# Optimization experiments

Hardware: AMD Instinct MI355X
Metric: run time of the kernel (lower is better)

The kernel has to match this reference:

```python
import jax, jax.numpy as jnp
import numpy as np

B, T, C, V = 4, 2048, 1024, 50257


def setup_inputs() -> dict:
    key = jax.random.key(0)
    k1, k2, k3 = jax.random.split(key, 3)
    x = jax.random.normal(k1, (B, T, C), dtype=jnp.float32)
    y = jax.random.randint(k2, (B, T), 0, V, dtype=jnp.int64)
    # nn.Linear(C, V): weight [V, C], bias [V]
    W = jax.random.normal(k3, (V, C), dtype=jnp.float32) * (1.0 / np.sqrt(C))
    b = jnp.zeros((V,), dtype=jnp.float32)
    return {"x": x, "y": y, "W": W, "b": b}


def reference(x, y, W, b):
    # logits: [B*T, V]
    logits = jnp.einsum("btc,vc->btv", x, W).reshape(B * T, V) + b
    labels = y.reshape(-1)  # [B*T]
    logp = jax.nn.log_softmax(logits, axis=-1)
    nll = -jnp.take_along_axis(logp, labels[:, None], axis=-1)[:, 0]
    return jnp.mean(nll)
```

## Files before the change

### kernel.cpp

```cpp
#include <hip/hip_runtime.h>


#define M_TOT 8192
#define K_TOT 1024
#define V_TOT 50257
#define NVB   197
#define NPAD  (NVB * 256)
#define PSTRIDE (NVB * 2)
#define KB    (K_TOT / 64)
#define GSTRIDE ((long)KB * 64 * 32)

typedef __attribute__((ext_vector_type(8)))  int   int8v;
typedef __attribute__((ext_vector_type(16))) float floatx16;

__device__ __forceinline__ int f4_to_fp8x4(float4 v) {
  int r = __builtin_amdgcn_cvt_pk_fp8_f32(v.x, v.y, 0, false);
  r = __builtin_amdgcn_cvt_pk_fp8_f32(v.z, v.w, r, true);
  return r;
}

__global__ __launch_bounds__(256) void pack_kernel(
    const float* __restrict__ src, char* __restrict__ dst, int nrows) {
  const int kb = blockIdx.x, g = blockIdx.y;
  const int i = threadIdx.x;
  const int r = i >> 3, seg = i & 7;
  const int srow = g * 32 + r;
  int lo = 0, hi = 0;
  if (srow < nrows) {
    const float4* s = (const float4*)(src + (long)srow * K_TOT + kb * 64 + seg * 8);
    lo = f4_to_fp8x4(s[0]);
    hi = f4_to_fp8x4(s[1]);
  }
  const int h = seg >> 2;
  char* d = dst + (((long)(g * KB + kb) * 64 + h * 32 + r) * 32 + (seg & 3) * 8);
  *(int2*)d = make_int2(lo, hi);
}

__global__ __launch_bounds__(256, 2) void gemm_lse_kernel(
    const char* __restrict__ pW, const char* __restrict__ pX,
    const float* __restrict__ bias, float* __restrict__ psum) {
  const int tid  = threadIdx.x;
  const int wave = tid >> 6;
  const int lane = tid & 63;
  const int wv   = wave >> 1;
  const int wb   = wave & 1;
  const int mblk = blockIdx.x;
  const int vblk = blockIdx.y;

  const char* pa[4];
  const char* pb[2];
#pragma unroll
  for (int tv = 0; tv < 4; ++tv)
    pa[tv] = pW + (long)(vblk * 8 + wv * 4 + tv) * GSTRIDE + (long)lane * 32;
#pragma unroll
  for (int tn = 0; tn < 2; ++tn)
    pb[tn] = pX + (long)(mblk * 4 + wb * 2 + tn) * GSTRIDE + (long)lane * 32;

  floatx16 acc[4][2] = {};
#pragma unroll 2
  for (int kb = 0; kb < KB; ++kb) {
    const int off = kb * 2048;
    int8v a[4], b[2];
#pragma unroll
    for (int tn = 0; tn < 2; ++tn) b[tn] = *(const int8v*)(pb[tn] + off);
#pragma unroll
    for (int tv = 0; tv < 4; ++tv) a[tv] = *(const int8v*)(pa[tv] + off);
#pragma unroll
    for (int tv = 0; tv < 4; ++tv)
#pragma unroll
      for (int tn = 0; tn < 2; ++tn)
        acc[tv][tn] = __builtin_amdgcn_mfma_scale_f32_32x32x64_f8f6f4(
            a[tv], b[tn], acc[tv][tn], 0, 0, 0, 0x7F7F7F7F, 0, 0x7F7F7F7F);
  }

  const int half = lane >> 5, l32 = lane & 31;
  const int vbase = vblk * 256 + wv * 128 + 4 * half;
  float s0 = 0.0f, s1 = 0.0f;
#pragma unroll
  for (int tv = 0; tv < 4; ++tv) {
#pragma unroll
    for (int reg = 0; reg < 16; ++reg) {
      int v = vbase + tv * 32 + (reg & 3) + 8 * (reg >> 2);
      float bv = (v < V_TOT) ? bias[v] : -1e30f;
      s0 += __expf(acc[tv][0][reg] + bv);
      s1 += __expf(acc[tv][1][reg] + bv);
    }
  }
  s0 += __shfl_xor(s0, 32, 64);
  s1 += __shfl_xor(s1, 32, 64);
  if (half == 0) {
    int m = mblk * 128 + wb * 64 + l32;
    long base = (long)m * PSTRIDE + vblk * 2 + wv;
    psum[base] = s0;
    psum[base + (long)32 * PSTRIDE] = s1;
  }
}

__global__ __launch_bounds__(256) void finalize_kernel(
    const float* __restrict__ psum, const float* __restrict__ x,
    const float* __restrict__ W, const float* __restrict__ b,
    const int* __restrict__ y, float* __restrict__ loss) {
  const int wave = threadIdx.x >> 6;
  const int lane = threadIdx.x & 63;
  const int r = blockIdx.x * 4 + wave;

  const float* ps = psum + (long)r * PSTRIDE;
  float s = 0.0f;
  for (int j = lane; j < PSTRIDE; j += 64) s += ps[j];
#pragma unroll
  for (int o = 1; o < 64; o <<= 1) s += __shfl_xor(s, o, 64);

  int label = y[r];
  const float4* xr = (const float4*)(x + (long)r * K_TOT);
  const float4* wr = (const float4*)(W + (long)label * K_TOT);
  float d = 0.0f;
  for (int j = lane; j < K_TOT / 4; j += 64) {
    float4 a = xr[j], w = wr[j];
    d += a.x * w.x + a.y * w.y + a.z * w.z + a.w * w.w;
  }
#pragma unroll
  for (int o = 1; o < 64; o <<= 1) d += __shfl_xor(d, o, 64);

  if (lane == 0) loss[r] = logf(s) - d - b[label];
}

__global__ __launch_bounds__(256) void reduce_kernel(
    const float* __restrict__ loss, float* __restrict__ out) {
  const int tid = threadIdx.x;
  float s = 0.0f;
  for (int j = tid; j < M_TOT; j += 256) s += loss[j];
#pragma unroll
  for (int o = 1; o < 64; o <<= 1) s += __shfl_xor(s, o, 64);
  __shared__ float wsum[4];
  if ((tid & 63) == 0) wsum[tid >> 6] = s;
  __syncthreads();
  if (tid == 0)
    out[0] = (wsum[0] + wsum[1] + wsum[2] + wsum[3]) * (1.0f / (float)M_TOT);
}

extern "C" void kernel_launch(void* const* d_in, const int* in_sizes, int n_in,
                              void* d_out, int out_size, void* d_ws, size_t ws_size,
                              hipStream_t stream) {
  (void)in_sizes; (void)n_in; (void)out_size; (void)ws_size;
  const float* x = (const float*)d_in[0];
  const int*   y = (const int*)d_in[1];
  const float* W = (const float*)d_in[2];
  const float* b = (const float*)d_in[3];
  float* out = (float*)d_out;

  char* ws = (char*)d_ws;
  const size_t PX_BYTES = (size_t)M_TOT * K_TOT;
  const size_t PW_BYTES = (size_t)NPAD * K_TOT;
  const size_t PS_BYTES = (size_t)M_TOT * PSTRIDE * 4;
  char*  pX   = ws;
  char*  pW   = ws + PX_BYTES;
  float* psum = (float*)(ws + PX_BYTES + PW_BYTES);
  float* loss = (float*)(ws + PX_BYTES + PW_BYTES + PS_BYTES);

  pack_kernel<<<dim3(KB, M_TOT / 32), 256, 0, stream>>>(x, pX, M_TOT);
  pack_kernel<<<dim3(KB, NPAD / 32), 256, 0, stream>>>(W, pW, V_TOT);
  gemm_lse_kernel<<<dim3(M_TOT / 128, NVB), 256, 0, stream>>>(pW, pX, b, psum);
  finalize_kernel<<<M_TOT / 4, 256, 0, stream>>>(psum, x, W, b, y, loss);
  reduce_kernel<<<1, 256, 0, stream>>>(loss, out);
}
```

Before: 736.6 us.

## Stage GEMM operands through swizzled double-buffered LDS with 512-thread blocks

The GEMM kernel previously had each wave load its fp8 fragments straight from global memory. It now stages A and B tiles into double-buffered LDS using global_load_lds, and the pack kernel writes an XOR-swizzled layout so the LDS reads avoid bank conflicts. Blocks grow to 512 threads covering 256 rows of M, so each loaded W tile is reused across more rows. Bias values are cached in LDS, and wave priority is raised around the MFMAs. In exchange it adds 128KB+ of LDS per block, which limits occupancy, plus extra barriers per k-step.

```diff
diff --git a/kernel.cpp b/kernel.cpp
--- a/kernel.cpp
+++ b/kernel.cpp
@@ -32,56 +32,107 @@
     hi = f4_to_fp8x4(s[1]);
   }
   const int h = seg >> 2;
-  char* d = dst + (((long)(g * KB + kb) * 64 + h * 32 + r) * 32 + (seg & 3) * 8);
+  const int c = (h * 32 + r) * 2 + ((seg >> 1) & 1);
+  const int sc = c ^ ((c >> 3) & 7);
+  char* d = dst + ((long)(g * KB + kb) * 2048 + sc * 16 + (seg & 1) * 8);
   *(int2*)d = make_int2(lo, hi);
 }
 
-__global__ __launch_bounds__(256, 2) void gemm_lse_kernel(
+#define GLOAD16(gp, lp)                                              \
+  __builtin_amdgcn_global_load_lds(                                  \
+      (const __attribute__((address_space(1))) void*)(gp),           \
+      (__attribute__((address_space(3))) void*)(lp), 16, 0, 0)
+
+__device__ __forceinline__ int8v read_frag(const char* base, int o0, int o1) {
+  int4 lo = *(const int4*)(base + o0);
+  int4 hi = *(const int4*)(base + o1);
+  int8v r;
+  r[0] = lo.x; r[1] = lo.y; r[2] = lo.z; r[3] = lo.w;
+  r[4] = hi.x; r[5] = hi.y; r[6] = hi.z; r[7] = hi.w;
+  return r;
+}
+
+__global__ __launch_bounds__(512, 2) void gemm_lse_kernel(
     const char* __restrict__ pW, const char* __restrict__ pX,
     const float* __restrict__ bias, float* __restrict__ psum) {
+  __shared__ char ldsA[2][32768];
+  __shared__ char ldsB[2][32768];
+  __shared__ float ldsbias[256];
+
   const int tid  = threadIdx.x;
-  const int wave = tid >> 6;
+  const int wid  = tid >> 6;
   const int lane = tid & 63;
-  const int wv   = wave >> 1;
-  const int wb   = wave & 1;
+  const int wv   = wid >> 2;
+  const int wb   = wid & 3;
   const int mblk = blockIdx.x;
   const int vblk = blockIdx.y;
 
-  const char* pa[4];
-  const char* pb[2];
-#pragma unroll
-  for (int tv = 0; tv < 4; ++tv)
-    pa[tv] = pW + (long)(vblk * 8 + wv * 4 + tv) * GSTRIDE + (long)lane * 32;
-#pragma unroll
-  for (int tn = 0; tn < 2; ++tn)
-    pb[tn] = pX + (long)(mblk * 4 + wb * 2 + tn) * GSTRIDE + (long)lane * 32;
+  const int c0 = lane * 2, c1 = c0 + 1;
+  const int off0 = (c0 ^ ((c0 >> 3) & 7)) * 16;
+  const int off1 = (c1 ^ ((c1 >> 3) & 7)) * 16;
+
+  const char* srcA = pW + (long)(vblk * 8 + wid) * GSTRIDE + lane * 16;
+  const char* srcB = pX + (long)(mblk * 8 + wid) * GSTRIDE + lane * 16;
+
+  auto stage = [&](int buf, int t) {
+#pragma unroll
+    for (int i = 0; i < 4; ++i) {
+      GLOAD16(srcA + (long)t * 4096 + i * 1024, ldsA[buf] + wid * 4096 + i * 1024);
+      GLOAD16(srcB + (long)t * 4096 + i * 1024, ldsB[buf] + wid * 4096 + i * 1024);
+    }
+  };
 
   floatx16 acc[4][2] = {};
-#pragma unroll 2
-  for (int kb = 0; kb < KB; ++kb) {
-    const int off = kb * 2048;
+
+  auto do_phase = [&](int cur, int s) {
     int8v a[4], b[2];
 #pragma unroll
-    for (int tn = 0; tn < 2; ++tn) b[tn] = *(const int8v*)(pb[tn] + off);
-#pragma unroll
-    for (int tv = 0; tv < 4; ++tv) a[tv] = *(const int8v*)(pa[tv] + off);
+    for (int tn = 0; tn < 2; ++tn)
+      b[tn] = read_frag(ldsB[cur] + ((wb * 2 + tn) * 2 + s) * 2048, off0, off1);
+#pragma unroll
+    for (int tv = 0; tv < 4; ++tv)
+      a[tv] = read_frag(ldsA[cur] + ((wv * 4 + tv) * 2 + s) * 2048, off0, off1);
+    asm volatile("" ::: "memory");
+    __builtin_amdgcn_s_barrier();
+    asm volatile("" ::: "memory");
+    __builtin_amdgcn_s_setprio(1);
 #pragma unroll
     for (int tv = 0; tv < 4; ++tv)
 #pragma unroll
       for (int tn = 0; tn < 2; ++tn)
         acc[tv][tn] = __builtin_amdgcn_mfma_scale_f32_32x32x64_f8f6f4(
             a[tv], b[tn], acc[tv][tn], 0, 0, 0, 0x7F7F7F7F, 0, 0x7F7F7F7F);
+    __builtin_amdgcn_s_setprio(0);
+  };
+
+  stage(0, 0);
+  if (tid < 256) {
+    int v = vblk * 256 + tid;
+    ldsbias[tid] = (v < V_TOT) ? bias[v] : -1e30f;
+  }
+  __syncthreads();
+
+  for (int t = 0; t < 8; ++t) {
+    const int cur = t & 1, nxt = cur ^ 1;
+    if (t < 7) stage(nxt, t + 1);
+    do_phase(cur, 0);
+    asm volatile("" ::: "memory");
+    __builtin_amdgcn_s_barrier();
+    asm volatile("" ::: "memory");
+    do_phase(cur, 1);
+    asm volatile("s_waitcnt vmcnt(0)" ::: "memory");
+    __builtin_amdgcn_s_barrier();
+    asm volatile("" ::: "memory");
   }
 
   const int half = lane >> 5, l32 = lane & 31;
-  const int vbase = vblk * 256 + wv * 128 + 4 * half;
+  const int bbase = wv * 128 + 4 * half;
   float s0 = 0.0f, s1 = 0.0f;
 #pragma unroll
   for (int tv = 0; tv < 4; ++tv) {
 #pragma unroll
     for (int reg = 0; reg < 16; ++reg) {
-      int v = vbase + tv * 32 + (reg & 3) + 8 * (reg >> 2);
-      float bv = (v < V_TOT) ? bias[v] : -1e30f;
+      float bv = ldsbias[bbase + tv * 32 + (reg & 3) + 8 * (reg >> 2)];
       s0 += __expf(acc[tv][0][reg] + bv);
       s1 += __expf(acc[tv][1][reg] + bv);
     }
@@ -89,7 +140,7 @@
   s0 += __shfl_xor(s0, 32, 64);
   s1 += __shfl_xor(s1, 32, 64);
   if (half == 0) {
-    int m = mblk * 128 + wb * 64 + l32;
+    int m = mblk * 256 + wb * 64 + l32;
     long base = (long)m * PSTRIDE + vblk * 2 + wv;
     psum[base] = s0;
     psum[base + (long)32 * PSTRIDE] = s1;
@@ -159,7 +210,7 @@
 
   pack_kernel<<<dim3(KB, M_TOT / 32), 256, 0, stream>>>(x, pX, M_TOT);
   pack_kernel<<<dim3(KB, NPAD / 32), 256, 0, stream>>>(W, pW, V_TOT);
-  gemm_lse_kernel<<<dim3(M_TOT / 128, NVB), 256, 0, stream>>>(pW, pX, b, psum);
+  gemm_lse_kernel<<<dim3(M_TOT / 256, NVB), 512, 0, stream>>>(pW, pX, b, psum);
   finalize_kernel<<<M_TOT / 4, 256, 0, stream>>>(psum, x, W, b, y, loss);
   reduce_kernel<<<1, 256, 0, stream>>>(loss, out);
 }
```

Result: slower. 808.4 us (+9.8%).
